# Performance work log

Measured on AMD Instinct MI355X. Metric: run time of the kernel, lower is better.

## Reference

```python
import jax, jax.numpy as jnp
import numpy as np

RADIUS = 9.0   # search_raduis_scale * particle_radius
K = 20         # N_neighbor
HIDDEN = [512, 512, 512, 512]


def embed(x, n_freqs):
    freqs = 2.0 ** jnp.arange(n_freqs, dtype=x.dtype)      # [F]
    xf = x[..., None, :] * freqs[:, None]                  # [..., F, C]
    sc = jnp.stack([jnp.sin(xf), jnp.cos(xf)], axis=-2)    # [..., F, 2, C]
    return jnp.concatenate([x, sc.reshape(*x.shape[:-1], -1)], axis=-1)


def ball_query(q, p, radius, k):
    # pytorch3d semantics: first k points (by index order) with squared dist < radius^2;
    # padding slots get dists=0, idx=-1, nn=0.
    n = p.shape[0]
    d2 = jnp.sum((q[:, None, :] - p[None, :, :]) ** 2, axis=-1)   # [P,N]
    valid = d2 < radius * radius
    score = jnp.where(valid, -jnp.arange(n, dtype=q.dtype), -jnp.inf)
    top, idx = jax.lax.top_k(score, k)                            # first k valid indices
    found = top > -jnp.inf
    safe = jnp.clip(idx, 0, n - 1)
    dists = jnp.where(found, jnp.take_along_axis(d2, safe, axis=1), 0.0)
    nn = jnp.where(found[..., None], p[safe], 0.0)                # [P,K,3]
    return dists, jnp.where(found, idx, -1), nn


def mlp(x, params):
    n = len(params)
    for l, (v, g, b) in enumerate(params):
        w = g * v / jnp.linalg.norm(v, axis=1, keepdims=True)     # weight_norm, dim=0
        x = x @ w.T + b
        if l < n - 1:
            x = jax.nn.relu(x)
    return jax.nn.sigmoid(x)


def setup_inputs() -> dict:
    key = jax.random.key(0)
    ks = jax.random.split(key, 32)
    R, S, N, F = 256, 128, 4096, 256
    P = R * S
    inp = {
        "points": jax.random.normal(ks[0], (P, 3), dtype=jnp.float32) * 3.0,
        "normals": jax.random.normal(ks[1], (P, 3), dtype=jnp.float32),
        "view_dirs": jax.random.normal(ks[2], (P, 3), dtype=jnp.float32),
        "feature_vectors": jax.random.normal(ks[3], (P, F), dtype=jnp.float32),
        "phys_points": jax.random.normal(ks[4], (N, 3), dtype=jnp.float32) * 3.0,
        "ray_dirs": jax.random.normal(ks[5], (R, 3), dtype=jnp.float32),
        "cam_loc": jax.random.normal(ks[6], (1, 3), dtype=jnp.float32),
    }
    d0 = 3 + 3 + 3 + F + 63 + 9 + 63 + 63 + 27 + 27   # = 517
    dims = [d0] + HIDDEN + [3]
    for l in range(len(dims) - 1):
        fan_in, fan_out = dims[l], dims[l + 1]
        inp[f"v{l}"] = jax.random.normal(ks[7 + l], (fan_out, fan_in), dtype=jnp.float32) * float(np.sqrt(2.0 / fan_out))
        inp[f"g{l}"] = jnp.ones((fan_out, 1), dtype=jnp.float32)
        inp[f"b{l}"] = jnp.zeros((fan_out,), dtype=jnp.float32)
    return inp


def reference(points, normals, view_dirs, feature_vectors, phys_points, ray_dirs, cam_loc,
              v0, g0, b0, v1, g1, b1, v2, g2, b2, v3, g3, b3, v4, g4, b4):
    params = [(v0, g0, b0), (v1, g1, b1), (v2, g2, b2), (v3, g3, b3), (v4, g4, b4)]
    # mode == 'idr'
    rendering_input = jnp.concatenate([points, view_dirs, normals, feature_vectors], axis=-1)
    dists, idx, neighbors = ball_query(points, phys_points, RADIUS, K)
    nn_mask = dists != 0                                             # [P,K]
    num_nn = nn_mask.sum(-1, keepdims=True).astype(points.dtype)     # [P,1]
    # smoothing_position (exclude_ray=True): Euclidean dists recomputed incl. zero-padded slots
    dd = jnp.linalg.norm(neighbors - points[:, None, :], axis=-1)    # [P,K]
    w = jnp.maximum(1.0 - (dd / RADIUS) ** 3, 0.0)
    smoothed_pos = (w[..., None] * neighbors).sum(-2) / (w.sum(-1, keepdims=True) + 1e-12)
    density = w.sum(-1, keepdims=True)                               # [P,1]
    d = smoothed_pos - cam_loc                                       # broadcast [P,3]
    smoothed_dir = d / jnp.linalg.norm(d, axis=-1, keepdims=True)
    # variance of masked neighbor offsets
    vec = jnp.where(nn_mask[..., None], neighbors - points[:, None, :], 0.0)
    vec_mean = vec.sum(-2) / (num_nn + 1e-12)                        # [P,3]
    var = jnp.where(nn_mask[..., None], (vec - vec_mean[:, None, :]) ** 2, 0.0).sum(-2) / (num_nn + 1e-12)
    reps = points.shape[0] // ray_dirs.shape[0]                      # samples per ray
    hit_dir_emb = jnp.repeat(embed(ray_dirs, 4), reps, axis=0)       # [P,27]
    feats = jnp.concatenate([embed(points, 10), embed(density, 4), embed(smoothed_pos, 10),
                             embed(var, 10), hit_dir_emb, embed(smoothed_dir, 4)], axis=-1)
    x = jnp.concatenate([rendering_input, feats], axis=-1)           # [P,517]
    return mlp(x, params)
```

## Files before the change

### kernel.cpp

```cpp
#include <hip/hip_runtime.h>
#include <hip/hip_bf16.h>

typedef unsigned short u16;
typedef short short8 __attribute__((ext_vector_type(8)));
typedef float f32x4 __attribute__((ext_vector_type(4)));

static __device__ __forceinline__ u16 f2bf(float f) {
  unsigned u = __builtin_bit_cast(unsigned, f);
  unsigned r = (u + 0x7fffu + ((u >> 16) & 1u)) >> 16;
  return (u16)r;
}
static __device__ __forceinline__ float bf2f(u16 h) {
  unsigned u = ((unsigned)h) << 16;
  return __builtin_bit_cast(float, u);
}

static __device__ __forceinline__ void gload_lds16(const u16* g, u16* l) {
  __builtin_amdgcn_global_load_lds(
      (const __attribute__((address_space(1))) void*)g,
      (__attribute__((address_space(3))) void*)l, 16, 0, 0);
}

__global__ void prep_w_bf16(const float* __restrict__ v, const float* __restrict__ g,
                            u16* __restrict__ out, int fan_in, int kpad) {
  const int row = blockIdx.x;
  const int lane = threadIdx.x;
  double s = 0.0;
  for (int k = lane; k < fan_in; k += 64) {
    double x = (double)v[(size_t)row * fan_in + k];
    s += x * x;
  }
#pragma unroll
  for (int off = 32; off; off >>= 1) s += __shfl_xor(s, off);
  double scale = (double)g[row] / sqrt(s);
  for (int k = lane; k < kpad; k += 64) {
    float wv = (k < fan_in) ? (float)((double)v[(size_t)row * fan_in + k] * scale) : 0.0f;
    out[(size_t)row * kpad + k] = f2bf(wv);
  }
}

__global__ void prep_w_f32(const float* __restrict__ v, const float* __restrict__ g,
                           float* __restrict__ out, int fan_in) {
  const int row = blockIdx.x;
  const int lane = threadIdx.x;
  double s = 0.0;
  for (int k = lane; k < fan_in; k += 64) {
    double x = (double)v[(size_t)row * fan_in + k];
    s += x * x;
  }
#pragma unroll
  for (int off = 32; off; off >>= 1) s += __shfl_xor(s, off);
  double scale = (double)g[row] / sqrt(s);
  for (int k = lane; k < fan_in; k += 64) {
    out[(size_t)row * fan_in + k] = (float)((double)v[(size_t)row * fan_in + k] * scale);
  }
}

__global__ __launch_bounds__(256) void scan_kernel(
    const float* __restrict__ pts, const float* __restrict__ phys,
    u16* __restrict__ idxbuf) {
  const int m = (int)((blockIdx.x * blockDim.x + threadIdx.x) >> 6);
  const int lane = (int)(threadIdx.x & 63);

  const double qx = (double)pts[m * 3 + 0];
  const double qy = (double)pts[m * 3 + 1];
  const double qz = (double)pts[m * 3 + 2];

  u16* __restrict__ row = idxbuf + (size_t)m * 24;

  int found = 0;
  for (int base = 0; base < 4096 && found < 20; base += 64) {
    const int j = base + lane;
    const double px = (double)phys[j * 3 + 0];
    const double py = (double)phys[j * 3 + 1];
    const double pz = (double)phys[j * 3 + 2];
    const double dx = px - qx, dy = py - qy, dz = pz - qz;
    const double d2 = dx * dx + dy * dy + dz * dz;
    const bool valid = d2 < 81.0;
    const unsigned long long mb = __ballot(valid);
    const int rank = found + __popcll(mb & ((1ull << lane) - 1ull));
    if (valid && rank < 20) row[rank] = (u16)j;
    found += __popcll(mb);
    if (found > 20) found = 20;
  }
  if (lane == 0) row[20] = (u16)found;
}

__global__ __launch_bounds__(256) void gstats_kernel(
    const float* __restrict__ pts, const float* __restrict__ phys,
    const float* __restrict__ cam, const u16* __restrict__ idxbuf,
    float* __restrict__ Pbuf) {
  const int i = blockIdx.x * 256 + threadIdx.x;

  const double qx = (double)pts[i * 3 + 0];
  const double qy = (double)pts[i * 3 + 1];
  const double qz = (double)pts[i * 3 + 2];

  const u16* __restrict__ row = idxbuf + (size_t)i * 24;
  const int cnt = (int)row[20];

  int nnn = 0;
  double w_sum = 0, wpx = 0, wpy = 0, wpz = 0;
  double Sx = 0, Sy = 0, Sz = 0, Qx = 0, Qy = 0, Qz = 0;

#pragma unroll
  for (int s = 0; s < 20; ++s) {
    if (s < cnt) {
      const int j = (int)row[s];
      const double px = (double)phys[j * 3 + 0];
      const double py = (double)phys[j * 3 + 1];
      const double pz = (double)phys[j * 3 + 2];
      const double dx = px - qx, dy = py - qy, dz = pz - qz;
      const double d2 = dx * dx + dy * dy + dz * dz;
      const float d2f = (float)d2;
      float wf = 1.0f - d2f * sqrtf(d2f) * (1.0f / 729.0f);
      if (wf < 0.0f) wf = 0.0f;
      const double w = (double)wf;
      w_sum += w; wpx += w * px; wpy += w * py; wpz += w * pz;
      if (d2 != 0.0) {
        nnn += 1;
        Sx += dx; Sy += dy; Sz += dz;
        Qx += dx * dx; Qy += dy * dy; Qz += dz * dz;
      }
    }
  }

  {
    const float q2f = (float)(qx * qx + qy * qy + qz * qz);
    float wpad = 1.0f - q2f * sqrtf(q2f) * (1.0f / 729.0f);
    if (wpad < 0.0f) wpad = 0.0f;
    w_sum += (double)(20 - cnt) * (double)wpad;
  }

  const double inv_denom = 1.0 / (w_sum + 1e-12);
  const double sposx = wpx * inv_denom, sposy = wpy * inv_denom, sposz = wpz * inv_denom;

  const double inv_nd = 1.0 / ((double)nnn + 1e-12);
  const double vmx = Sx * inv_nd, vmy = Sy * inv_nd, vmz = Sz * inv_nd;
  const float vax = (float)((Qx - 2.0 * vmx * Sx + (double)nnn * vmx * vmx) * inv_nd);
  const float vay = (float)((Qy - 2.0 * vmy * Sy + (double)nnn * vmy * vmy) * inv_nd);
  const float vaz = (float)((Qz - 2.0 * vmz * Sz + (double)nnn * vmz * vmz) * inv_nd);

  const double ddx = sposx - (double)cam[0];
  const double ddy = sposy - (double)cam[1];
  const double ddz = sposz - (double)cam[2];
  const double inv_dnm = 1.0 / sqrt(ddx * ddx + ddy * ddy + ddz * ddz);

  f32x4* out = (f32x4*)(Pbuf + (size_t)i * 12);
  f32x4 o0, o1, o2;
  o0[0] = (float)w_sum; o0[1] = (float)sposx; o0[2] = (float)sposy; o0[3] = (float)sposz;
  o1[0] = vax; o1[1] = vay; o1[2] = vaz; o1[3] = (float)(ddx * inv_dnm);
  o2[0] = (float)(ddy * inv_dnm); o2[1] = (float)(ddz * inv_dnm); o2[2] = 0.0f; o2[3] = 0.0f;
  out[0] = o0; out[1] = o1; out[2] = o2;
}

__global__ void build_plan(unsigned* __restrict__ plan) {
  const int k = blockIdx.x * 64 + threadIdx.x;
  if (k >= 576) return;
  unsigned p;
  if (k < 9) {
    p = (unsigned)k;
  } else if (k < 265) {
    p = 3u << 8;
  } else if (k >= 328 && k < 337) {
    int e = k - 328;
    if (e == 0) p = 9u;
    else {
      int u = e - 1;
      p = 9u | (((u & 1) ? 2u : 1u) << 8) | ((unsigned)(u >> 1) << 12);
    }
  } else if (k < 517) {
    int e, src0;
    if (k < 328)      { e = k - 265; src0 = 0;  }
    else if (k < 400) { e = k - 337; src0 = 10; }
    else if (k < 463) { e = k - 400; src0 = 13; }
    else if (k < 490) { e = k - 463; src0 = 16; }
    else              { e = k - 490; src0 = 19; }
    if (e < 3) p = (unsigned)(src0 + e);
    else {
      int u = e - 3, f = u / 6, r = u - f * 6, ci = r % 3;
      p = (unsigned)(src0 + ci) | (((r < 3) ? 1u : 2u) << 8) | ((unsigned)f << 12);
    }
  } else {
    p = 4u << 8;
  }
  plan[k] = p;
}

__global__ __launch_bounds__(256) void emb_kernel(
    const float* __restrict__ pts, const float* __restrict__ nrm,
    const float* __restrict__ vdir, const float* __restrict__ fv,
    const float* __restrict__ rdir, const float* __restrict__ Pbuf,
    const unsigned* __restrict__ plan, u16* __restrict__ X) {
  const int m = (int)((blockIdx.x * blockDim.x + threadIdx.x) >> 6);
  const int lane = (int)(threadIdx.x & 63);
  const int wv = (int)(threadIdx.x >> 6);

  __shared__ float sc[4][24];
  if (lane < 3) {
    const int ray = m >> 7;
    sc[wv][lane] = pts[m * 3 + lane];
    sc[wv][3 + lane] = vdir[m * 3 + lane];
    sc[wv][6 + lane] = nrm[m * 3 + lane];
    sc[wv][16 + lane] = rdir[ray * 3 + lane];
  }
  if (lane < 10) {
    sc[wv][lane < 7 ? 9 + lane : 12 + lane] = Pbuf[(size_t)m * 12 + lane];
  }
  __syncthreads();

  u16* __restrict__ xrow = X + (size_t)m * 576;
#pragma unroll
  for (int it = 0; it < 9; ++it) {
    const int k = it * 64 + lane;
    const unsigned p = plan[k];
    const unsigned op = (p >> 8) & 7u;
    float val;
    if (op == 3u) {
      val = fv[(size_t)m * 256 + (k - 9)];
    } else if (op == 4u) {
      val = 0.0f;
    } else {
      float x = sc[wv][p & 31u];
      x *= __builtin_bit_cast(float, (127u + ((p >> 12) & 31u)) << 23);
      if (op == 0u) {
        val = x;
      } else {
        float r = x * 0.15915494309189535f;
        if (op == 2u) r += 0.25f;
        r -= floorf(r);
        val = __builtin_amdgcn_sinf(r);
      }
    }
    xrow[k] = f2bf(val);
  }
}

template <int KTILES>
__global__ __launch_bounds__(256) void gemm_relu(const u16* __restrict__ A,
                                                 const u16* __restrict__ B,
                                                 const float* __restrict__ bias,
                                                 u16* __restrict__ C) {
  constexpr int K = KTILES * 64;
  __shared__ __align__(16) u16 As[2][128][64];
  __shared__ __align__(16) u16 Bs[2][128][64];

  const int t = threadIdx.x;
  const int lane = t & 63;
  const int wid = t >> 6;
  const int wm = wid >> 1, wn = wid & 1;

  const int bid = blockIdx.x;
  const int wgid = (bid & 7) * 128 + (bid >> 3);
  const int n0 = (wgid & 3) * 128;
  const int m0 = (wgid >> 2) * 128;

  const int srow = lane >> 3;
  const int gcol = ((lane & 7) ^ srow) * 8;

  f32x4 acc[4][4] = {};

#define STAGE(kt, b)                                                            \
  {                                                                             \
    const int k0_ = (kt) * 64;                                                  \
    _Pragma("unroll")                                                           \
    for (int i_ = 0; i_ < 4; ++i_) {                                            \
      const int rbase_ = wid * 32 + i_ * 8;                                     \
      const int row_ = rbase_ + srow;                                           \
      gload_lds16(A + (size_t)(m0 + row_) * K + k0_ + gcol, &As[b][rbase_][0]); \
      gload_lds16(B + (size_t)(n0 + row_) * K + k0_ + gcol, &Bs[b][rbase_][0]); \
    }                                                                           \
  }

  STAGE(0, 0);

  const int rsw = lane & 7;
  for (int kt = 0; kt < KTILES; ++kt) {
    const int cur = kt & 1;
    __builtin_amdgcn_s_barrier();
    if (kt + 1 < KTILES) {
      STAGE(kt + 1, cur ^ 1);
      asm volatile("s_waitcnt vmcnt(8)" ::: "memory");
    } else {
      asm volatile("s_waitcnt vmcnt(0)" ::: "memory");
    }
    __builtin_amdgcn_s_barrier();
#pragma unroll
    for (int ks = 0; ks < 2; ++ks) {
      short8 af[4], bfv[4];
#pragma unroll
      for (int f = 0; f < 4; ++f) {
        const int ar = wm * 64 + f * 16 + (lane & 15);
        const int br = wn * 64 + f * 16 + (lane & 15);
        const int cc = ((ks * 4 + (lane >> 4)) ^ rsw) * 8;
        af[f]  = *(const short8*)&As[cur][ar][cc];
        bfv[f] = *(const short8*)&Bs[cur][br][cc];
      }
#pragma unroll
      for (int fm = 0; fm < 4; ++fm)
#pragma unroll
        for (int fn = 0; fn < 4; ++fn)
          acc[fm][fn] = __builtin_amdgcn_mfma_f32_16x16x32_bf16(af[fm], bfv[fn], acc[fm][fn], 0, 0, 0);
    }
  }
#undef STAGE

  const int lr = lane >> 4, lc = lane & 15;
#pragma unroll
  for (int fn = 0; fn < 4; ++fn) {
    const int col = n0 + wn * 64 + fn * 16 + lc;
    const float bv = bias[col];
#pragma unroll
    for (int fm = 0; fm < 4; ++fm) {
      const int rowb = m0 + wm * 64 + fm * 16 + lr * 4;
#pragma unroll
      for (int rg = 0; rg < 4; ++rg) {
        float vv = acc[fm][fn][rg] + bv;
        vv = fmaxf(vv, 0.0f);
        C[(size_t)(rowb + rg) * 512 + col] = f2bf(vv);
      }
    }
  }
}

__global__ __launch_bounds__(256) void final_kernel(const u16* __restrict__ H,
                                                    const float* __restrict__ W4,
                                                    const float* __restrict__ b4,
                                                    float* __restrict__ out) {
  const int m = (int)((blockIdx.x * blockDim.x + threadIdx.x) >> 6);
  const int lane = (int)(threadIdx.x & 63);

  short8 hv = *(const short8*)(H + (size_t)m * 512 + lane * 8);
  float x[8];
#pragma unroll
  for (int e = 0; e < 8; ++e) x[e] = bf2f((u16)hv[e]);

  float s0 = 0, s1 = 0, s2 = 0;
  const float* w0 = W4 + 0 * 512 + lane * 8;
  const float* w1 = W4 + 1 * 512 + lane * 8;
  const float* w2 = W4 + 2 * 512 + lane * 8;
#pragma unroll
  for (int e = 0; e < 8; ++e) {
    s0 += x[e] * w0[e];
    s1 += x[e] * w1[e];
    s2 += x[e] * w2[e];
  }
#pragma unroll
  for (int off = 32; off; off >>= 1) {
    s0 += __shfl_xor(s0, off);
    s1 += __shfl_xor(s1, off);
    s2 += __shfl_xor(s2, off);
  }
  if (lane < 3) {
    float v = (lane == 0) ? s0 : (lane == 1 ? s1 : s2);
    v += b4[lane];
    out[(size_t)m * 3 + lane] = 1.0f / (1.0f + expf(-v));
  }
}

extern "C" void kernel_launch(void* const* d_in, const int* in_sizes, int n_in,
                              void* d_out, int out_size, void* d_ws, size_t ws_size,
                              hipStream_t stream) {
  const float* pts  = (const float*)d_in[0];
  const float* nrm  = (const float*)d_in[1];
  const float* vdir = (const float*)d_in[2];
  const float* fv   = (const float*)d_in[3];
  const float* phys = (const float*)d_in[4];
  const float* rdir = (const float*)d_in[5];
  const float* cam  = (const float*)d_in[6];
  const float* v0 = (const float*)d_in[7];  const float* g0 = (const float*)d_in[8];  const float* b0 = (const float*)d_in[9];
  const float* v1 = (const float*)d_in[10]; const float* g1 = (const float*)d_in[11]; const float* b1 = (const float*)d_in[12];
  const float* v2 = (const float*)d_in[13]; const float* g2 = (const float*)d_in[14]; const float* b2 = (const float*)d_in[15];
  const float* v3 = (const float*)d_in[16]; const float* g3 = (const float*)d_in[17]; const float* b3 = (const float*)d_in[18];
  const float* v4 = (const float*)d_in[19]; const float* g4 = (const float*)d_in[20]; const float* b4 = (const float*)d_in[21];

  char* ws = (char*)d_ws;
  u16*      W0 = (u16*)(ws + 0);
  u16*      W1 = (u16*)(ws + 589824);
  u16*      W2 = (u16*)(ws + 1114112);
  u16*      W3 = (u16*)(ws + 1638400);
  float*    W4 = (float*)(ws + 2162688);
  unsigned* Pl = (unsigned*)(ws + 2168832);
  u16*      Ix = (u16*)(ws + 2171136);
  float*    Pb = (float*)(ws + 3744000);
  u16*      X  = (u16*)(ws + 5316864);
  u16*      H1 = (u16*)(ws + 43065600);
  u16*      H2 = X;

  prep_w_bf16<<<512, 64, 0, stream>>>(v0, g0, W0, 517, 576);
  prep_w_bf16<<<512, 64, 0, stream>>>(v1, g1, W1, 512, 512);
  prep_w_bf16<<<512, 64, 0, stream>>>(v2, g2, W2, 512, 512);
  prep_w_bf16<<<512, 64, 0, stream>>>(v3, g3, W3, 512, 512);
  prep_w_f32<<<3, 64, 0, stream>>>(v4, g4, W4, 512);
  build_plan<<<9, 64, 0, stream>>>(Pl);

  scan_kernel<<<8192, 256, 0, stream>>>(pts, phys, Ix);
  gstats_kernel<<<128, 256, 0, stream>>>(pts, phys, cam, Ix, Pb);
  emb_kernel<<<8192, 256, 0, stream>>>(pts, nrm, vdir, fv, rdir, Pb, Pl, X);

  gemm_relu<9><<<1024, 256, 0, stream>>>(X,  W0, b0, H1);
  gemm_relu<8><<<1024, 256, 0, stream>>>(H1, W1, b1, H2);
  gemm_relu<8><<<1024, 256, 0, stream>>>(H2, W2, b2, H1);
  gemm_relu<8><<<1024, 256, 0, stream>>>(H1, W3, b3, H2);

  final_kernel<<<8192, 256, 0, stream>>>(H2, W4, b4, (float*)d_out);
}
```

Measured before the change: 180.9 us.

## Permute layer-0 input columns so embedding writes 16-byte vectorized chunks

```diff
diff --git a/kernel.cpp b/kernel.cpp
--- a/kernel.cpp
+++ b/kernel.cpp
@@ -3,6 +3,7 @@
 
 typedef unsigned short u16;
 typedef short short8 __attribute__((ext_vector_type(8)));
+typedef unsigned short ushort8 __attribute__((ext_vector_type(8)));
 typedef float f32x4 __attribute__((ext_vector_type(4)));
 
 static __device__ __forceinline__ u16 f2bf(float f) {
@@ -19,6 +20,47 @@
   __builtin_amdgcn_global_load_lds(
       (const __attribute__((address_space(1))) void*)g,
       (__attribute__((address_space(3))) void*)l, 16, 0, 0);
+}
+
+
+__global__ void prep_w0(const float* __restrict__ v, const float* __restrict__ g,
+                        u16* __restrict__ out) {
+  const int row = blockIdx.x;
+  const int lane = threadIdx.x;
+  double s = 0.0;
+  for (int k = lane; k < 517; k += 64) {
+    double x = (double)v[(size_t)row * 517 + k];
+    s += x * x;
+  }
+#pragma unroll
+  for (int off = 32; off; off >>= 1) s += __shfl_xor(s, off);
+  double scale = (double)g[row] / sqrt(s);
+
+  for (int j = lane; j < 576; j += 64) {
+    int orig = -1;
+    if (j < 256) {
+      orig = 9 + j;
+    } else if (j < 281) {
+      int e = j - 256;
+      if (e < 9)       orig = e;
+      else if (e < 12) orig = 265 + (e - 9);
+      else if (e == 12) orig = 328;
+      else if (e < 16) orig = 337 + (e - 13);
+      else if (e < 19) orig = 400 + (e - 16);
+      else if (e < 22) orig = 463 + (e - 19);
+      else if (e < 25) orig = 490 + (e - 22);
+    } else if (j >= 288 && j < 524) {
+      int t = j - 288;
+      if (t < 60)       orig = 268 + t;
+      else if (t < 68)  orig = 329 + (t - 60);
+      else if (t < 128) orig = 340 + (t - 68);
+      else if (t < 188) orig = 403 + (t - 128);
+      else if (t < 212) orig = 466 + (t - 188);
+      else if (t < 236) orig = 493 + (t - 212);
+    }
+    float wv = (orig >= 0) ? (float)((double)v[(size_t)row * 517 + orig] * scale) : 0.0f;
+    out[(size_t)row * 576 + j] = f2bf(wv);
+  }
 }
 
 __global__ void prep_w_bf16(const float* __restrict__ v, const float* __restrict__ g,
@@ -54,6 +96,42 @@
   for (int k = lane; k < fan_in; k += 64) {
     out[(size_t)row * fan_in + k] = (float)((double)v[(size_t)row * fan_in + k] * scale);
   }
+}
+
+__global__ void build_tb(u16* __restrict__ TB) {
+  const int i = blockIdx.x * 64 + threadIdx.x;
+  if (i >= 320) return;
+  const int j = 256 + i;
+  unsigned d = 0;
+  if (j < 281) {
+    int e = j - 256;
+    int src = -1;
+    if (e < 9)       src = e;
+    else if (e < 12) src = e - 9;
+    else if (e == 12) src = 9;
+    else if (e < 16) src = 10 + (e - 13);
+    else if (e < 19) src = 13 + (e - 16);
+    else if (e < 22) src = 16 + (e - 19);
+    else if (e < 25) src = 19 + (e - 22);
+    if (src >= 0) d = 1u | ((unsigned)src << 2);
+  } else if (j >= 288 && j < 524) {
+    int t = j - 288;
+    if (t < 236) {
+      int base, src0;
+      if (t < 60)       { base = 0;   src0 = 0;  }
+      else if (t < 68)  { base = 60;  src0 = 9;  }
+      else if (t < 128) { base = 68;  src0 = 10; }
+      else if (t < 188) { base = 128; src0 = 13; }
+      else if (t < 212) { base = 188; src0 = 16; }
+      else              { base = 212; src0 = 19; }
+      int u = t - base;
+      int f, cs, src;
+      if (src0 == 9) { f = u >> 1; cs = u & 1; src = 9; }
+      else { f = u / 6; int r = u - 6 * f; cs = (r >= 3) ? 1 : 0; src = src0 + (cs ? r - 3 : r); }
+      d = 2u | ((unsigned)src << 2) | ((unsigned)cs << 7) | ((unsigned)f << 8);
+    }
+  }
+  TB[i] = (u16)d;
 }
 
 __global__ __launch_bounds__(256) void scan_kernel(
@@ -154,85 +232,63 @@
   out[0] = o0; out[1] = o1; out[2] = o2;
 }
 
-__global__ void build_plan(unsigned* __restrict__ plan) {
-  const int k = blockIdx.x * 64 + threadIdx.x;
-  if (k >= 576) return;
-  unsigned p;
-  if (k < 9) {
-    p = (unsigned)k;
-  } else if (k < 265) {
-    p = 3u << 8;
-  } else if (k >= 328 && k < 337) {
-    int e = k - 328;
-    if (e == 0) p = 9u;
-    else {
-      int u = e - 1;
-      p = 9u | (((u & 1) ? 2u : 1u) << 8) | ((unsigned)(u >> 1) << 12);
-    }
-  } else if (k < 517) {
-    int e, src0;
-    if (k < 328)      { e = k - 265; src0 = 0;  }
-    else if (k < 400) { e = k - 337; src0 = 10; }
-    else if (k < 463) { e = k - 400; src0 = 13; }
-    else if (k < 490) { e = k - 463; src0 = 16; }
-    else              { e = k - 490; src0 = 19; }
-    if (e < 3) p = (unsigned)(src0 + e);
-    else {
-      int u = e - 3, f = u / 6, r = u - f * 6, ci = r % 3;
-      p = (unsigned)(src0 + ci) | (((r < 3) ? 1u : 2u) << 8) | ((unsigned)f << 12);
-    }
-  } else {
-    p = 4u << 8;
-  }
-  plan[k] = p;
-}
-
-__global__ __launch_bounds__(256) void emb_kernel(
+__global__ __launch_bounds__(576) void emb_kernel(
     const float* __restrict__ pts, const float* __restrict__ nrm,
     const float* __restrict__ vdir, const float* __restrict__ fv,
     const float* __restrict__ rdir, const float* __restrict__ Pbuf,
-    const unsigned* __restrict__ plan, u16* __restrict__ X) {
-  const int m = (int)((blockIdx.x * blockDim.x + threadIdx.x) >> 6);
-  const int lane = (int)(threadIdx.x & 63);
-  const int wv = (int)(threadIdx.x >> 6);
-
-  __shared__ float sc[4][24];
-  if (lane < 3) {
-    const int ray = m >> 7;
-    sc[wv][lane] = pts[m * 3 + lane];
-    sc[wv][3 + lane] = vdir[m * 3 + lane];
-    sc[wv][6 + lane] = nrm[m * 3 + lane];
-    sc[wv][16 + lane] = rdir[ray * 3 + lane];
-  }
-  if (lane < 10) {
-    sc[wv][lane < 7 ? 9 + lane : 12 + lane] = Pbuf[(size_t)m * 12 + lane];
+    const u16* __restrict__ TB, u16* __restrict__ X) {
+  const int cc = (int)threadIdx.x;
+  const int y = (int)threadIdx.y;
+  const int m = blockIdx.x * 8 + y;
+
+  __shared__ float sc[8][24];
+  if (cc < 22) {
+    float v;
+    if (cc < 3)       v = pts[m * 3 + cc];
+    else if (cc < 6)  v = vdir[m * 3 + (cc - 3)];
+    else if (cc < 9)  v = nrm[m * 3 + (cc - 6)];
+    else if (cc < 10) v = Pbuf[(size_t)m * 12 + 0];
+    else if (cc < 13) v = Pbuf[(size_t)m * 12 + 1 + (cc - 10)];
+    else if (cc < 16) v = Pbuf[(size_t)m * 12 + 4 + (cc - 13)];
+    else if (cc < 19) v = rdir[(m >> 7) * 3 + (cc - 16)];
+    else              v = Pbuf[(size_t)m * 12 + 7 + (cc - 19)];
+    sc[y][cc] = v;
   }
   __syncthreads();
 
-  u16* __restrict__ xrow = X + (size_t)m * 576;
-#pragma unroll
-  for (int it = 0; it < 9; ++it) {
-    const int k = it * 64 + lane;
-    const unsigned p = plan[k];
-    const unsigned op = (p >> 8) & 7u;
-    float val;
-    if (op == 3u) {
-      val = fv[(size_t)m * 256 + (k - 9)];
-    } else if (op == 4u) {
-      val = 0.0f;
-    } else {
-      float x = sc[wv][p & 31u];
-      x *= __builtin_bit_cast(float, (127u + ((p >> 12) & 31u)) << 23);
-      if (op == 0u) {
-        val = x;
-      } else {
-        float r = x * 0.15915494309189535f;
-        if (op == 2u) r += 0.25f;
-        r -= floorf(r);
-        val = __builtin_amdgcn_sinf(r);
+  u16* __restrict__ xp = X + (size_t)m * 576 + cc * 8;
+
+  if (cc < 32) {
+    const f32x4* fp = (const f32x4*)(fv + (size_t)m * 256 + cc * 8);
+    f32x4 a = fp[0], b = fp[1];
+    short8 o;
+    o[0] = (short)f2bf(a[0]); o[1] = (short)f2bf(a[1]);
+    o[2] = (short)f2bf(a[2]); o[3] = (short)f2bf(a[3]);
+    o[4] = (short)f2bf(b[0]); o[5] = (short)f2bf(b[1]);
+    o[6] = (short)f2bf(b[2]); o[7] = (short)f2bf(b[3]);
+    *(short8*)xp = o;
+  } else {
+    ushort8 tb = *(const ushort8*)(TB + (size_t)(cc - 32) * 8);
+    short8 o;
+#pragma unroll
+    for (int e = 0; e < 8; ++e) {
+      const unsigned d = (unsigned)tb[e];
+      const unsigned kind = d & 3u;
+      float val = 0.0f;
+      if (kind) {
+        float x = sc[y][(d >> 2) & 31u];
+        if (kind == 2u) {
+          x *= __builtin_bit_cast(float, (127u + (d >> 8)) << 23);
+          float r = x * 0.15915494309189535f + (((d >> 7) & 1u) ? 0.25f : 0.0f);
+          r -= floorf(r);
+          val = __builtin_amdgcn_sinf(r);
+        } else {
+          val = x;
+        }
       }
-    }
-    xrow[k] = f2bf(val);
+      o[e] = (short)f2bf(val);
+    }
+    *(short8*)xp = o;
   }
 }
 
@@ -380,23 +436,23 @@
   u16*      W2 = (u16*)(ws + 1114112);
   u16*      W3 = (u16*)(ws + 1638400);
   float*    W4 = (float*)(ws + 2162688);
-  unsigned* Pl = (unsigned*)(ws + 2168832);
+  u16*      TB = (u16*)(ws + 2168832);
   u16*      Ix = (u16*)(ws + 2171136);
   float*    Pb = (float*)(ws + 3744000);
   u16*      X  = (u16*)(ws + 5316864);
   u16*      H1 = (u16*)(ws + 43065600);
   u16*      H2 = X;
 
-  prep_w_bf16<<<512, 64, 0, stream>>>(v0, g0, W0, 517, 576);
+  prep_w0<<<512, 64, 0, stream>>>(v0, g0, W0);
   prep_w_bf16<<<512, 64, 0, stream>>>(v1, g1, W1, 512, 512);
   prep_w_bf16<<<512, 64, 0, stream>>>(v2, g2, W2, 512, 512);
   prep_w_bf16<<<512, 64, 0, stream>>>(v3, g3, W3, 512, 512);
   prep_w_f32<<<3, 64, 0, stream>>>(v4, g4, W4, 512);
-  build_plan<<<9, 64, 0, stream>>>(Pl);
+  build_tb<<<5, 64, 0, stream>>>(TB);
 
   scan_kernel<<<8192, 256, 0, stream>>>(pts, phys, Ix);
   gstats_kernel<<<128, 256, 0, stream>>>(pts, phys, cam, Ix, Pb);
-  emb_kernel<<<8192, 256, 0, stream>>>(pts, nrm, vdir, fv, rdir, Pb, Pl, X);
+  emb_kernel<<<4096, dim3(72, 8), 0, stream>>>(pts, nrm, vdir, fv, rdir, Pb, TB, X);
 
   gemm_relu<9><<<1024, 256, 0, stream>>>(X,  W0, b0, H1);
   gemm_relu<8><<<1024, 256, 0, stream>>>(H1, W1, b1, H2);
```

After: 177.6 us. Within noise of the previous version (-1.8%).
